# Performance work log

Measured on AMD Instinct MI355X. Metric: run time of the kernel, lower is better.

Reference implementation:

```python
import jax, jax.numpy as jnp
import numpy as np
import math

D_MODEL = 512
N_HEADS = 8
D_K = D_MODEL // N_HEADS
B, S, KC = 16, 1024, 32
NEG = -1e32


def setup_inputs() -> dict:
    key = jax.random.key(0)
    ks = jax.random.split(key, 14)
    s = 1.0 / math.sqrt(D_MODEL)
    return {
        "q": jax.random.normal(ks[0], (B, S, D_MODEL), jnp.float32),
        "k": jax.random.normal(ks[1], (B, S, D_MODEL), jnp.float32),
        "v": jax.random.normal(ks[2], (B, S, D_MODEL), jnp.float32),
        "q_seq": jax.random.randint(ks[3], (B, S), 0, 500, jnp.int32),
        "c_seq": jax.random.randint(ks[4], (B, S, KC), 0, 2, jnp.int32),
        "Wq": jax.random.normal(ks[5], (D_MODEL, D_MODEL), jnp.float32) * s,
        "bq": jnp.zeros((D_MODEL,), jnp.float32),
        "Wk": jax.random.normal(ks[6], (D_MODEL, D_MODEL), jnp.float32) * s,
        "bk": jnp.zeros((D_MODEL,), jnp.float32),
        "Wv": jax.random.normal(ks[7], (D_MODEL, D_MODEL), jnp.float32) * s,
        "bv": jnp.zeros((D_MODEL,), jnp.float32),
        "Wo": jax.random.normal(ks[8], (D_MODEL, D_MODEL), jnp.float32) * s,
        "bo": jnp.zeros((D_MODEL,), jnp.float32),
    }


def qc_mask(q_seq, c_seq):
    # maskq[b,i,j] = 1 if same question id
    maskq = (q_seq[:, :, None] == q_seq[:, None, :]).astype(jnp.int32)
    # maskc[b,i,j] = 1 if any shared concept; entries are {0,1} so AND-sum == dot
    overlap = jnp.einsum("bik,bjk->bij", c_seq, c_seq)  # int32
    maskc = (overlap > 0).astype(jnp.int32)
    # strict lower triangle: 1 - triu(ones, k=0)
    tri = jnp.tril(jnp.ones((S, S), jnp.int32), k=-1)[None]
    return (maskc + maskq + 1) * tri  # values in {0,1,2,3}


def reference(q, k, v, q_seq, c_seq, Wq, bq, Wk, bk, Wv, bv, Wo, bo):
    bs = q.shape[0]
    # NOTE: original code swaps the linears: k<-k_linear(k), q<-v_linear(q), v<-q_linear(v)
    kh = (k @ Wk.T + bk).reshape(bs, S, N_HEADS, D_K).transpose(0, 2, 1, 3)
    qh = (q @ Wv.T + bv).reshape(bs, S, N_HEADS, D_K).transpose(0, 2, 1, 3)
    vh = (v @ Wq.T + bq).reshape(bs, S, N_HEADS, D_K).transpose(0, 2, 1, 3)

    mask = qc_mask(q_seq, c_seq)  # [B,S,S] int
    scores = jnp.einsum("bhid,bhjd->bhij", qh, kh) / math.sqrt(D_K)
    m = mask[:, None]  # [B,1,S,S]
    scores = jnp.where(m == 0, NEG, scores)
    scores = jax.nn.softmax(scores, axis=-1)

    adjustments = jnp.array([0.0, 0.5, 1.0, 2.0], jnp.float32)
    adjusted = scores * adjustments[m]
    sums = jnp.sum(scores, axis=-1, keepdims=True)
    sums = jnp.where(sums == 0, jnp.ones_like(sums), sums)
    adjusted = adjusted / sums

    out = jnp.einsum("bhij,bhjd->bhid", adjusted, vh)
    concat = out.transpose(0, 2, 1, 3).reshape(bs, S, D_MODEL)
    return concat @ Wo.T + bo
```

## Files before the change

kernel.cpp:

```cpp
#include <hip/hip_runtime.h>
#include <stdint.h>

typedef unsigned short u16;
typedef unsigned int   u32;
typedef unsigned long long u64;
typedef __attribute__((ext_vector_type(8)))  short short8;
typedef __attribute__((ext_vector_type(4)))  float f32x4;
typedef __attribute__((ext_vector_type(16))) float f32x16;
typedef __attribute__((ext_vector_type(4)))  unsigned int u32x4;

__device__ __forceinline__ u16 f2bf(float f) {
  u32 u = __builtin_bit_cast(u32, f);
  u32 r = u + 0x7FFFu + ((u >> 16) & 1u);
  return (u16)(r >> 16);
}

__device__ __forceinline__ u32 cvtpk(float a, float b) {
  u32 r;
  asm("v_cvt_pk_bf16_f32 %0, %1, %2" : "=v"(r) : "v"(a), "v"(b));
  return r;
}

__device__ __forceinline__ void gload_lds16(const void* g, void* l) {
  __builtin_amdgcn_global_load_lds(
      (__attribute__((address_space(1))) void*)(uintptr_t)g,
      (__attribute__((address_space(3))) void*)(u32)(uintptr_t)l,
      16, 0, 0);
}

__global__ void cast4_kernel(const float* __restrict__ s0, const float* __restrict__ s1,
                             const float* __restrict__ s2, const float* __restrict__ s3,
                             u16* __restrict__ d0, u16* __restrict__ d1,
                             u16* __restrict__ d2, u16* __restrict__ d3, int n8) {
  const int sel = blockIdx.y;
  const float* src = sel == 0 ? s0 : sel == 1 ? s1 : sel == 2 ? s2 : s3;
  u16* dst = sel == 0 ? d0 : sel == 1 ? d1 : sel == 2 ? d2 : d3;
  int i = blockIdx.x * blockDim.x + threadIdx.x;
  if (i >= n8) return;
  const float4* s4 = (const float4*)src;
  float4 x = s4[2 * (size_t)i];
  float4 y = s4[2 * (size_t)i + 1];
  u32x4 r;
  r.x = cvtpk(x.x, x.y); r.y = cvtpk(x.z, x.w);
  r.z = cvtpk(y.x, y.y); r.w = cvtpk(y.z, y.w);
  *(u32x4*)(dst + 8 * (size_t)i) = r;
}

__global__ void pack_kernel(const int* __restrict__ q_seq, const int* __restrict__ c_seq,
                            int2* __restrict__ meta, int n) {
  int i = blockIdx.x * blockDim.x + threadIdx.x;
  if (i >= n) return;
  u32 bits = 0;
#pragma unroll
  for (int j = 0; j < 32; ++j)
    bits |= (c_seq[(size_t)i * 32 + j] != 0) ? (1u << j) : 0u;
  meta[i] = make_int2(q_seq[i], (int)bits);
}

__global__ __launch_bounds__(256) void mask_kernel(const int2* __restrict__ meta,
                                                   u64* __restrict__ maskw) {
  const int qc = blockIdx.x, kt = blockIdx.y, b = blockIdx.z;
  const int t = threadIdx.x;
  const int q = qc * 256 + t;
  __shared__ int2 colm[32];
  if (t < 32) colm[t] = meta[b * 1024 + kt * 32 + t];
  __syncthreads();
  const int2 qm = meta[b * 1024 + q];
  const int rs = qm.x; const u32 rb = (u32)qm.y;
  u64 w = 0;
#pragma unroll
  for (int j = 0; j < 32; ++j) {
    const int2 cm = colm[j];
    const int kj = kt * 32 + j;
    u32 m = 0;
    if (kj < q) m = 1u + (rs == cm.x ? 1u : 0u) + (((rb & (u32)cm.y) != 0u) ? 1u : 0u);
    w |= (u64)m << (2 * j);
  }
  maskw[((size_t)b * 32 + kt) * 1024 + q] = w;
}

__global__ __launch_bounds__(256) void gemm_qkv(const float* __restrict__ qf,
                                                const float* __restrict__ kf,
                                                const float* __restrict__ vf,
                                                const u16* __restrict__ Wvb,
                                                const u16* __restrict__ Wkb,
                                                const u16* __restrict__ Wqb,
                                                const float* __restrict__ bv,
                                                const float* __restrict__ bk,
                                                const float* __restrict__ bq,
                                                u16* __restrict__ qhb,
                                                u16* __restrict__ khb,
                                                u16* __restrict__ vTb,
                                                float kscale) {
  const int sel = blockIdx.y;
  const float* Af   = sel == 0 ? qf : sel == 1 ? kf : vf;
  const u16*   W    = sel == 0 ? Wvb : sel == 1 ? Wkb : Wqb;
  const float* bias = sel == 0 ? bv : sel == 1 ? bk : bq;
  const float scale = sel == 1 ? kscale : 1.0f;
  const int K = 512, N = 512;

  __shared__ __align__(16) u16 As[128 * 64];
  __shared__ __align__(16) u16 Bs[128 * 64];
  const int t    = threadIdx.x;
  const int lane = t & 63;
  const int wid  = t >> 6;
  const int g    = lane >> 4, l15 = lane & 15;
  const int wm   = wid >> 1, wn = wid & 1;
  const int mb   = blockIdx.x >> 2, nbi = blockIdx.x & 3;
  const int m0   = mb << 7, n0 = nbi << 7;
  const int srow = t >> 3;
  const int scol = (t & 7) << 3;

  f32x4 acc[4][4];
#pragma unroll
  for (int i = 0; i < 4; ++i)
#pragma unroll
    for (int j = 0; j < 4; ++j) acc[i][j] = f32x4{0.f, 0.f, 0.f, 0.f};

  for (int k0 = 0; k0 < K; k0 += 64) {
    __syncthreads();
#pragma unroll
    for (int i = 0; i < 4; ++i) {
      const u16* sb = W + (size_t)(n0 + i * 32 + srow) * K + k0 + scol;
      gload_lds16(sb, Bs + i * 2048 + t * 8);
    }
#pragma unroll
    for (int i = 0; i < 4; ++i) {
      const float* src = Af + (size_t)(m0 + 32 * i + srow) * K + k0 + scol;
      const float4 x = *(const float4*)src;
      const float4 y = *(const float4*)(src + 4);
      u32x4 r;
      r.x = cvtpk(x.x, x.y); r.y = cvtpk(x.z, x.w);
      r.z = cvtpk(y.x, y.y); r.w = cvtpk(y.z, y.w);
      *(u32x4*)(As + (32 * i + srow) * 64 + scol) = r;
    }
    __syncthreads();
#pragma unroll
    for (int kk = 0; kk < 2; ++kk) {
      short8 a[4], b[4];
#pragma unroll
      for (int mi = 0; mi < 4; ++mi)
        a[mi] = *(const short8*)(As + (wm * 64 + mi * 16 + l15) * 64 + kk * 32 + g * 8);
#pragma unroll
      for (int ni = 0; ni < 4; ++ni)
        b[ni] = *(const short8*)(Bs + (wn * 64 + ni * 16 + l15) * 64 + kk * 32 + g * 8);
#pragma unroll
      for (int mi = 0; mi < 4; ++mi)
#pragma unroll
        for (int ni = 0; ni < 4; ++ni)
          acc[mi][ni] = __builtin_amdgcn_mfma_f32_16x16x32_bf16(a[mi], b[ni], acc[mi][ni], 0, 0, 0);
    }
  }

#pragma unroll
  for (int ni = 0; ni < 4; ++ni) {
    const int col = n0 + wn * 64 + ni * 16 + l15;
    const float bz = bias[col];
#pragma unroll
    for (int mi = 0; mi < 4; ++mi) {
#pragma unroll
      for (int r = 0; r < 4; ++r) {
        const int row = m0 + wm * 64 + mi * 16 + g * 4 + r;
        const u16 val = f2bf((acc[mi][ni][r] + bz) * scale);
        const size_t base = ((size_t)(row >> 10) * 8 + (col >> 6)) * 65536;
        const int s = row & 1023, d = col & 63;
        if (sel == 0) {
          qhb[base + (size_t)s * 64 + d] = val;
        } else if (sel == 1) {
          khb[base + (s >> 5) * 2048 + (d >> 3) * 256 + (s & 31) * 8 + (d & 7)] = val;
        } else {
          vTb[base + (s >> 3) * 512 + d * 8 + (s & 7)] = val;
        }
      }
    }
  }
}

__global__ __launch_bounds__(256) void gemm_out(const u16* __restrict__ A,
                                                const u16* __restrict__ W,
                                                const float* __restrict__ bias,
                                                float* __restrict__ outp) {
  const int K = 512, N = 512;
  __shared__ __align__(16) u16 As[128 * 64];
  __shared__ __align__(16) u16 Bs[128 * 64];
  const int t    = threadIdx.x;
  const int lane = t & 63;
  const int wid  = t >> 6;
  const int g    = lane >> 4, l15 = lane & 15;
  const int wm   = wid >> 1, wn = wid & 1;
  const int mb   = blockIdx.x >> 2, nbi = blockIdx.x & 3;
  const int m0   = mb << 7, n0 = nbi << 7;
  const int srow = t >> 3;
  const int scol = (t & 7) << 3;

  f32x4 acc[4][4];
#pragma unroll
  for (int i = 0; i < 4; ++i)
#pragma unroll
    for (int j = 0; j < 4; ++j) acc[i][j] = f32x4{0.f, 0.f, 0.f, 0.f};

  for (int k0 = 0; k0 < K; k0 += 64) {
    __syncthreads();
#pragma unroll
    for (int i = 0; i < 4; ++i) {
      const u16* sa = A + (size_t)(m0 + i * 32 + srow) * K + k0 + scol;
      const u16* sb = W + (size_t)(n0 + i * 32 + srow) * K + k0 + scol;
      gload_lds16(sa, As + i * 2048 + t * 8);
      gload_lds16(sb, Bs + i * 2048 + t * 8);
    }
    __syncthreads();
#pragma unroll
    for (int kk = 0; kk < 2; ++kk) {
      short8 a[4], b[4];
#pragma unroll
      for (int mi = 0; mi < 4; ++mi)
        a[mi] = *(const short8*)(As + (wm * 64 + mi * 16 + l15) * 64 + kk * 32 + g * 8);
#pragma unroll
      for (int ni = 0; ni < 4; ++ni)
        b[ni] = *(const short8*)(Bs + (wn * 64 + ni * 16 + l15) * 64 + kk * 32 + g * 8);
#pragma unroll
      for (int mi = 0; mi < 4; ++mi)
#pragma unroll
        for (int ni = 0; ni < 4; ++ni)
          acc[mi][ni] = __builtin_amdgcn_mfma_f32_16x16x32_bf16(a[mi], b[ni], acc[mi][ni], 0, 0, 0);
    }
  }

#pragma unroll
  for (int ni = 0; ni < 4; ++ni) {
    const int col = n0 + wn * 64 + ni * 16 + l15;
    const float bz = bias[col];
#pragma unroll
    for (int mi = 0; mi < 4; ++mi)
#pragma unroll
      for (int r = 0; r < 4; ++r) {
        const int row = m0 + wm * 64 + mi * 16 + g * 4 + r;
        outp[(size_t)row * N + col] = acc[mi][ni][r] + bz;
      }
  }
}

__global__ __launch_bounds__(256, 4) void attn_kernel(const u16* __restrict__ qh,
                                                      const u16* __restrict__ kh,
                                                      const u16* __restrict__ vT,
                                                      const u64* __restrict__ maskw,
                                                      u16* __restrict__ outc) {
  const int h  = blockIdx.x;
  const int qp = blockIdx.y;
  const int b  = blockIdx.z;
  const int lane = threadIdx.x & 63;
  const int wid  = threadIdx.x >> 6;
  const int pair = wid >> 1, p = wid & 1;
  const int l31 = lane & 31;
  const int hh  = lane >> 5;
  const int hh8 = hh << 3, fourh = hh << 2, eighth = hh << 3;
  const int jt = pair ? (31 - qp) : qp;
  const int q0 = jt << 5;
  const int qi = q0 + l31;
  const size_t bh = (size_t)b * 8 + h;
  const u16* Q  = qh + bh * 65536;
  const u16* Kp = kh + bh * 65536;
  const u16* Vt = vT + bh * 65536;
  const u64* mrow = maskw + (size_t)b * 32768 + qi;

  __shared__ float mO[2][32][64];
  __shared__ float mL[2][64];
  __shared__ __align__(16) float Sl[2][32];

  short8 qB[4];
#pragma unroll
  for (int i = 0; i < 4; ++i)
    qB[i] = *(const short8*)(Q + (size_t)qi * 64 + i * 16 + eighth);

  f32x16 O0, O1;
#pragma unroll
  for (int i = 0; i < 16; ++i) { O0[i] = 0.f; O1[i] = 0.f; }
  float lr[4] = {0.f, 0.f, 0.f, 0.f};

  const int nt = jt + 1;

  short8 kA[4];
#pragma unroll
  for (int i = 0; i < 4; ++i)
    kA[i] = *(const short8*)(Kp + p * 2048 + ((2 * i + hh) * 32 + l31) * 8);
  u64 wm = mrow[(size_t)p << 10];

  for (int t = p; t < nt; t += 2) {
    const int k0 = t << 5;

    f32x16 S;
#pragma unroll
    for (int i = 0; i < 16; ++i) S[i] = 0.f;
#pragma unroll
    for (int i = 0; i < 4; ++i)
      S = __builtin_amdgcn_mfma_f32_32x32x16_bf16(kA[i], qB[i], S, 0, 0, 0);

    u64 wmn = 0;
    if (t + 2 < nt) {
#pragma unroll
      for (int i = 0; i < 4; ++i)
        kA[i] = *(const short8*)(Kp + (t + 2) * 2048 + ((2 * i + hh) * 32 + l31) * 8);
      wmn = mrow[(size_t)(t + 2) << 10];
    }

    short8 vB[2][2];
#pragma unroll
    for (int t4 = 0; t4 < 2; ++t4)
#pragma unroll
      for (int j = 0; j < 2; ++j)
        vB[t4][j] = *(const short8*)(Vt + (size_t)(t * 4 + t4 * 2 + hh) * 512 + (32 * j + l31) * 8);

    const u32 wsh0 = ((u32)wm) >> hh8;
    const u32 wsh1 = ((u32)(wm >> 32)) >> hh8;
    u32 pk[8];
#pragma unroll
    for (int s = 0; s < 4; ++s) {
      const u32 wsel = (s < 2) ? wsh0 : wsh1;
      float pv[4];
#pragma unroll
      for (int r = 0; r < 4; ++r) {
        const int m = 4 * s + r;
        const u32 m2 = (wsel >> (2 * r + 16 * (s & 1))) & 3u;
        float e;
        asm("v_exp_f32 %0, %1" : "=v"(e) : "v"(S[m]));
        const float pp = (m2 != 0u) ? e : 0.f;
        lr[r] += pp;
        asm("v_ldexp_f32 %0, %1, %2" : "=v"(pv[r]) : "v"(pp), "v"(m2));
      }
      pk[2 * s]     = cvtpk(pv[0], pv[1]);
      pk[2 * s + 1] = cvtpk(pv[2], pv[3]);
    }
    wm = wmn;

#pragma unroll
    for (int t4 = 0; t4 < 2; ++t4) {
      u32 a0 = pk[4 * t4 + 0], b0 = pk[4 * t4 + 2];
      u32 a1 = pk[4 * t4 + 1], b1 = pk[4 * t4 + 3];
      asm("v_permlane32_swap_b32 %0, %1" : "+v"(a0), "+v"(b0));
      asm("v_permlane32_swap_b32 %0, %1" : "+v"(a1), "+v"(b1));
      u32x4 w; w.x = a0; w.y = a1; w.z = b0; w.w = b1;
      const short8 pa = __builtin_bit_cast(short8, w);
      O0 = __builtin_amdgcn_mfma_f32_32x32x16_bf16(pa, vB[t4][0], O0, 0, 0, 0);
      O1 = __builtin_amdgcn_mfma_f32_32x32x16_bf16(pa, vB[t4][1], O1, 0, 0, 0);
    }
  }

  float lrun = (lr[0] + lr[1]) + (lr[2] + lr[3]);

  if (p == 1) {
#pragma unroll
    for (int r = 0; r < 16; ++r) {
      mO[pair][r][lane]      = O0[r];
      mO[pair][16 + r][lane] = O1[r];
    }
    mL[pair][lane] = lrun;
  }
  __syncthreads();
  if (p == 0) {
#pragma unroll
    for (int r = 0; r < 16; ++r) {
      O0[r] += mO[pair][r][lane];
      O1[r] += mO[pair][16 + r][lane];
    }
    lrun += mL[pair][lane];

    const float ssum = lrun + __shfl_xor(lrun, 32);
    if (lane < 32) Sl[pair][l31] = (ssum > 0.f) ? 0.25f / ssum : 0.f;
    __builtin_amdgcn_sched_barrier(0);
    asm volatile("s_waitcnt lgkmcnt(0)" ::: "memory");
    __builtin_amdgcn_sched_barrier(0);
#pragma unroll
    for (int t2 = 0; t2 < 4; ++t2) {
      const float4 inv4 = *(const float4*)&Sl[pair][8 * t2 + fourh];
#pragma unroll
      for (int r = 0; r < 4; ++r) {
        const int m = 4 * t2 + r;
        const float iv = (r == 0) ? inv4.x : (r == 1) ? inv4.y : (r == 2) ? inv4.z : inv4.w;
        const int qrow = q0 + 8 * t2 + fourh + r;
        u16* op = outc + ((size_t)b * 1024 + qrow) * 512 + h * 64;
        op[l31]      = f2bf(O0[m] * iv);
        op[32 + l31] = f2bf(O1[m] * iv);
      }
    }
  }
}

extern "C" void kernel_launch(void* const* d_in, const int* in_sizes, int n_in,
                              void* d_out, int out_size, void* d_ws, size_t ws_size,
                              hipStream_t stream) {
  (void)in_sizes; (void)n_in; (void)out_size; (void)ws_size;
  const float* q    = (const float*)d_in[0];
  const float* k    = (const float*)d_in[1];
  const float* v    = (const float*)d_in[2];
  const int*  q_seq = (const int*)d_in[3];
  const int*  c_seq = (const int*)d_in[4];
  const float* Wq   = (const float*)d_in[5];
  const float* bq   = (const float*)d_in[6];
  const float* Wk   = (const float*)d_in[7];
  const float* bk   = (const float*)d_in[8];
  const float* Wv   = (const float*)d_in[9];
  const float* bv   = (const float*)d_in[10];
  const float* Wo   = (const float*)d_in[11];
  const float* bo   = (const float*)d_in[12];
  float* out = (float*)d_out;

  char* ws = (char*)d_ws;
  const size_t SZH = 16ull * 8 * 1024 * 64 * 2;
  u16* qhb   = (u16*)(ws + 0 * SZH);
  u16* khb   = (u16*)(ws + 1 * SZH);
  u16* vTb   = (u16*)(ws + 2 * SZH);
  u16* attnc = (u16*)(ws + 3 * SZH);
  u16* Wvb = (u16*)(ws + 4 * SZH + 0 * 524288);
  u16* Wkb = (u16*)(ws + 4 * SZH + 1 * 524288);
  u16* Wqb = (u16*)(ws + 4 * SZH + 2 * 524288);
  u16* Wob = (u16*)(ws + 4 * SZH + 3 * 524288);
  int2* meta  = (int2*)(ws + 4 * SZH + 4 * 524288);
  u64* maskw  = (u64*)(ws + 4 * SZH + 4 * 524288 + 131072);

  const int n8w = 512 * 512 / 8;
  cast4_kernel<<<dim3(n8w / 256, 4), 256, 0, stream>>>(Wv, Wk, Wq, Wo,
                                                       Wvb, Wkb, Wqb, Wob, n8w);
  pack_kernel<<<64, 256, 0, stream>>>(q_seq, c_seq, meta, 16384);
  mask_kernel<<<dim3(4, 32, 16), 256, 0, stream>>>(meta, maskw);

  const float KSCALE = 0.18033688011112042f;
  gemm_qkv<<<dim3(512, 3), 256, 0, stream>>>(q, k, v, Wvb, Wkb, Wqb,
                                             bv, bk, bq, qhb, khb, vTb, KSCALE);
  attn_kernel<<<dim3(8, 16, 16), 256, 0, stream>>>(qhb, khb, vTb, maskw, attnc);
  gemm_out<<<512, 256, 0, stream>>>(attnc, Wob, bo, out);
}
```

Measured before the change: 170.0 us.

## Swizzle LDS tiles, remap block order, and prefetch A in QKV GEMM

Both projection GEMMs now XOR-swizzle the LDS column chunk by row, on the global source side for the direct-to-LDS loads and on the read side for MFMA fragments, to cut LDS bank conflicts. Block indices are remapped so neighbouring blocks share weight and activation tiles, which should help cache reuse. The QKV GEMM also prefetches the next K-slice of fp32 activations into registers while the current tile is being computed, and uses explicit barriers and waitcnts in place of __syncthreads. This adds register pressure and relies on hand-placed waitcnt values being correct.

```diff
diff --git a/kernel.cpp b/kernel.cpp
--- a/kernel.cpp
+++ b/kernel.cpp
@@ -97,7 +97,7 @@
   const u16*   W    = sel == 0 ? Wvb : sel == 1 ? Wkb : Wqb;
   const float* bias = sel == 0 ? bv : sel == 1 ? bk : bq;
   const float scale = sel == 1 ? kscale : 1.0f;
-  const int K = 512, N = 512;
+  const int K = 512;
 
   __shared__ __align__(16) u16 As[128 * 64];
   __shared__ __align__(16) u16 Bs[128 * 64];
@@ -106,10 +106,12 @@
   const int wid  = t >> 6;
   const int g    = lane >> 4, l15 = lane & 15;
   const int wm   = wid >> 1, wn = wid & 1;
-  const int mb   = blockIdx.x >> 2, nbi = blockIdx.x & 3;
+  const int wrk  = (blockIdx.x & 7) * 64 + (blockIdx.x >> 3);
+  const int mb   = wrk >> 2, nbi = wrk & 3;
   const int m0   = mb << 7, n0 = nbi << 7;
   const int srow = t >> 3;
-  const int scol = (t & 7) << 3;
+  const int scol = (((t & 7) ^ (srow & 7)) << 3);
+  const int rsw  = l15 & 7;
 
   f32x4 acc[4][4];
 #pragma unroll
@@ -117,33 +119,52 @@
 #pragma unroll
     for (int j = 0; j < 4; ++j) acc[i][j] = f32x4{0.f, 0.f, 0.f, 0.f};
 
+  float4 ax[4], ay[4];
+#pragma unroll
+  for (int i = 0; i < 4; ++i) {
+    const float* src = Af + (size_t)(m0 + 32 * i + srow) * K + scol;
+    ax[i] = *(const float4*)src;
+    ay[i] = *(const float4*)(src + 4);
+  }
+
   for (int k0 = 0; k0 < K; k0 += 64) {
-    __syncthreads();
+    __builtin_amdgcn_sched_barrier(0);
+    __builtin_amdgcn_s_barrier();
+    __builtin_amdgcn_sched_barrier(0);
+#pragma unroll
+    for (int i = 0; i < 4; ++i)
+      gload_lds16(W + (size_t)(n0 + i * 32 + srow) * K + k0 + scol,
+                  Bs + i * 2048 + t * 8);
 #pragma unroll
     for (int i = 0; i < 4; ++i) {
-      const u16* sb = W + (size_t)(n0 + i * 32 + srow) * K + k0 + scol;
-      gload_lds16(sb, Bs + i * 2048 + t * 8);
-    }
+      u32x4 r;
+      r.x = cvtpk(ax[i].x, ax[i].y); r.y = cvtpk(ax[i].z, ax[i].w);
+      r.z = cvtpk(ay[i].x, ay[i].y); r.w = cvtpk(ay[i].z, ay[i].w);
+      *(u32x4*)(As + (32 * i + srow) * 64 + ((t & 7) << 3)) = r;
+    }
+    __builtin_amdgcn_sched_barrier(0);
+    const int kn = (k0 + 64) & (K - 1);
 #pragma unroll
     for (int i = 0; i < 4; ++i) {
-      const float* src = Af + (size_t)(m0 + 32 * i + srow) * K + k0 + scol;
-      const float4 x = *(const float4*)src;
-      const float4 y = *(const float4*)(src + 4);
-      u32x4 r;
-      r.x = cvtpk(x.x, x.y); r.y = cvtpk(x.z, x.w);
-      r.z = cvtpk(y.x, y.y); r.w = cvtpk(y.z, y.w);
-      *(u32x4*)(As + (32 * i + srow) * 64 + scol) = r;
-    }
-    __syncthreads();
+      const float* src = Af + (size_t)(m0 + 32 * i + srow) * K + kn + scol;
+      ax[i] = *(const float4*)src;
+      ay[i] = *(const float4*)(src + 4);
+    }
+    __builtin_amdgcn_sched_barrier(0);
+    asm volatile("s_waitcnt vmcnt(8) lgkmcnt(0)" ::: "memory");
+    __builtin_amdgcn_s_barrier();
+    __builtin_amdgcn_sched_barrier(0);
 #pragma unroll
     for (int kk = 0; kk < 2; ++kk) {
       short8 a[4], b[4];
 #pragma unroll
       for (int mi = 0; mi < 4; ++mi)
-        a[mi] = *(const short8*)(As + (wm * 64 + mi * 16 + l15) * 64 + kk * 32 + g * 8);
+        a[mi] = *(const short8*)(As + (wm * 64 + mi * 16 + l15) * 64
+                                 + (((kk * 4 + g) ^ rsw) << 3));
 #pragma unroll
       for (int ni = 0; ni < 4; ++ni)
-        b[ni] = *(const short8*)(Bs + (wn * 64 + ni * 16 + l15) * 64 + kk * 32 + g * 8);
+        b[ni] = *(const short8*)(Bs + (wn * 64 + ni * 16 + l15) * 64
+                                 + (((kk * 4 + g) ^ rsw) << 3));
 #pragma unroll
       for (int mi = 0; mi < 4; ++mi)
 #pragma unroll
@@ -151,6 +172,7 @@
           acc[mi][ni] = __builtin_amdgcn_mfma_f32_16x16x32_bf16(a[mi], b[ni], acc[mi][ni], 0, 0, 0);
     }
   }
+  asm volatile("s_waitcnt vmcnt(0)" ::: "memory");
 
 #pragma unroll
   for (int ni = 0; ni < 4; ++ni) {
@@ -188,10 +210,12 @@
   const int wid  = t >> 6;
   const int g    = lane >> 4, l15 = lane & 15;
   const int wm   = wid >> 1, wn = wid & 1;
-  const int mb   = blockIdx.x >> 2, nbi = blockIdx.x & 3;
+  const int wrk  = (blockIdx.x & 7) * 64 + (blockIdx.x >> 3);
+  const int mb   = wrk >> 2, nbi = wrk & 3;
   const int m0   = mb << 7, n0 = nbi << 7;
   const int srow = t >> 3;
-  const int scol = (t & 7) << 3;
+  const int scol = (((t & 7) ^ (srow & 7)) << 3);
+  const int rsw  = l15 & 7;
 
   f32x4 acc[4][4];
 #pragma unroll
@@ -200,24 +224,29 @@
     for (int j = 0; j < 4; ++j) acc[i][j] = f32x4{0.f, 0.f, 0.f, 0.f};
 
   for (int k0 = 0; k0 < K; k0 += 64) {
-    __syncthreads();
+    __builtin_amdgcn_sched_barrier(0);
+    __builtin_amdgcn_s_barrier();
+    __builtin_amdgcn_sched_barrier(0);
 #pragma unroll
     for (int i = 0; i < 4; ++i) {
-      const u16* sa = A + (size_t)(m0 + i * 32 + srow) * K + k0 + scol;
-      const u16* sb = W + (size_t)(n0 + i * 32 + srow) * K + k0 + scol;
-      gload_lds16(sa, As + i * 2048 + t * 8);
-      gload_lds16(sb, Bs + i * 2048 + t * 8);
-    }
-    __syncthreads();
+      gload_lds16(A + (size_t)(m0 + i * 32 + srow) * K + k0 + scol, As + i * 2048 + t * 8);
+      gload_lds16(W + (size_t)(n0 + i * 32 + srow) * K + k0 + scol, Bs + i * 2048 + t * 8);
+    }
+    __builtin_amdgcn_sched_barrier(0);
+    asm volatile("s_waitcnt vmcnt(0)" ::: "memory");
+    __builtin_amdgcn_s_barrier();
+    __builtin_amdgcn_sched_barrier(0);
 #pragma unroll
     for (int kk = 0; kk < 2; ++kk) {
       short8 a[4], b[4];
 #pragma unroll
       for (int mi = 0; mi < 4; ++mi)
-        a[mi] = *(const short8*)(As + (wm * 64 + mi * 16 + l15) * 64 + kk * 32 + g * 8);
+        a[mi] = *(const short8*)(As + (wm * 64 + mi * 16 + l15) * 64
+                                 + (((kk * 4 + g) ^ rsw) << 3));
 #pragma unroll
       for (int ni = 0; ni < 4; ++ni)
-        b[ni] = *(const short8*)(Bs + (wn * 64 + ni * 16 + l15) * 64 + kk * 32 + g * 8);
+        b[ni] = *(const short8*)(Bs + (wn * 64 + ni * 16 + l15) * 64
+                                 + (((kk * 4 + g) ^ rsw) << 3));
 #pragma unroll
       for (int mi = 0; mi < 4; ++mi)
 #pragma unroll
```

New measurement: 142.6 us. 16.2% less time.
